# Optimization experiments

Hardware: AMD Instinct MI355X
Metric: run time of the kernel (lower is better)

The kernel has to match this reference:

```python
import jax, jax.numpy as jnp
import numpy as np

B, LS, LT = 64, 64, 64
E, H = 512, 512
VS, VT = 32000, 32000


def setup_inputs() -> dict:
    key = jax.random.key(0)
    ks = jax.random.split(key, 16)
    s = 0.02
    inp = {
        "src": jax.random.randint(ks[0], (B, LS), 0, VS),
        "tgt": jax.random.randint(ks[1], (B, LT), 0, VT),
        # encoder params
        "src_embed": jax.random.normal(ks[2], (VS, E), jnp.float32) * s,
        "enc_Wx": jax.random.normal(ks[3], (E, 4 * H), jnp.float32) * s,   # [i|f|g|o]
        "enc_Wh": jax.random.normal(ks[4], (H, 4 * H), jnp.float32) * s,
        "enc_b": jnp.zeros((4 * H,), jnp.float32),
        # decoder params
        "tgt_embed": jax.random.normal(ks[5], (VT, E), jnp.float32) * s,
        "att_Wh": jax.random.normal(ks[6], (H, H), jnp.float32) * s,
        "att_Ws": jax.random.normal(ks[7], (H, H), jnp.float32) * s,
        "att_v": jax.random.normal(ks[8], (H,), jnp.float32) * s,
        "dec_Wx": jax.random.normal(ks[9], (E + H, 4 * H), jnp.float32) * s,
        "dec_Wh": jax.random.normal(ks[10], (H, 4 * H), jnp.float32) * s,
        "dec_b": jnp.zeros((4 * H,), jnp.float32),
        "h2o_W": jax.random.normal(ks[11], (2 * H, VT), jnp.float32) * s,
        "h2o_b": jnp.zeros((VT,), jnp.float32),
    }
    return inp


def _lstm_step(x, h, c, Wx, Wh, b):
    # x:(B,in), h,c:(B,H). Gates packed as [i|f|g|o] along last dim (same math
    # as 8 separate nn.Linear calls with biases summed).
    z = x @ Wx + h @ Wh + b
    i, f, g, o = jnp.split(z, 4, axis=-1)
    c_new = jax.nn.sigmoid(f) * c + jax.nn.sigmoid(i) * jnp.tanh(g)
    h_new = jax.nn.sigmoid(o) * jnp.tanh(c_new)
    return h_new, c_new


def reference(src, tgt, src_embed, enc_Wx, enc_Wh, enc_b, tgt_embed,
              att_Wh, att_Ws, att_v, dec_Wx, dec_Wh, dec_b, h2o_W, h2o_b):
    Bs = src.shape[0]
    h0 = jnp.zeros((Bs, H), jnp.float32)
    c0 = jnp.zeros((Bs, H), jnp.float32)

    # ---- encoder: scan over source timesteps ----
    src_emb = src_embed[src]                       # (B,Ls,E)
    xs_enc = jnp.swapaxes(src_emb, 0, 1)           # (Ls,B,E)

    def enc_step(carry, x):
        h, c = carry
        h, c = _lstm_step(x, h, c, enc_Wx, enc_Wh, enc_b)
        return (h, c), h

    (h_enc, c_enc), enc_hs = jax.lax.scan(enc_step, (h0, c0), xs_enc)
    enc_hiddens = jnp.swapaxes(enc_hs, 0, 1)       # (B,Ls,H)

    # encoder-side attention projection is decoder-state independent: hoist it
    enc_t = enc_hiddens @ att_Wh                   # (B,Ls,H)

    # ---- decoder: teacher forcing, scan over target timesteps ----
    tgt_emb = tgt_embed[tgt]                       # (B,Lt,E)
    xs_dec = jnp.swapaxes(tgt_emb, 0, 1)           # (Lt,B,E)

    def dec_step(carry, emb):
        h, c = carry
        # Bahdanau additive attention on previous decoder hidden h
        dec_t = h @ att_Ws                                        # (B,H)
        energy = jnp.tanh(enc_t + dec_t[:, None, :]) @ att_v      # (B,Ls)
        attn = jax.nn.softmax(energy, axis=-1)                    # (B,Ls)
        context = jnp.einsum('bs,bsh->bh', attn, enc_hiddens)     # (B,H)
        lstm_in = jnp.concatenate([emb, context], axis=-1)        # (B,E+H)
        h, c = _lstm_step(lstm_in, h, c, dec_Wx, dec_Wh, dec_b)
        logits = jnp.concatenate([h, context], axis=-1) @ h2o_W + h2o_b
        out = jax.nn.log_softmax(logits, axis=-1)                 # (B,Vt)
        return (h, c), out

    _, outs = jax.lax.scan(dec_step, (h_enc, c_enc), xs_dec)      # (Lt,B,Vt)
    return jnp.swapaxes(outs, 0, 1)                               # (B,Lt,Vt)
```

## Files before the change

### kernel.cpp

```cpp
#include <hip/hip_runtime.h>
#include <hip/hip_bf16.h>
#include <math.h>

#define BB 64
#define LL 64
#define EE 512
#define HH 512
#define G4 2048
#define VT 32000
#define RT 4096

typedef unsigned short u16;
typedef unsigned int u32;
typedef unsigned char u8;
typedef __attribute__((ext_vector_type(2))) unsigned int u32x2;
typedef __attribute__((ext_vector_type(8))) unsigned short ushort8;
typedef __attribute__((ext_vector_type(8))) short bf16x8;
typedef __attribute__((ext_vector_type(4))) float f32x4;

__device__ u16   gW2T[(size_t)VT * 1024];
__device__ u16   gEncWxT[G4 * EE];
__device__ u16   gEncWhT[G4 * HH];
__device__ u16   gAttWhT[HH * HH];
__device__ u16   gDecWxTe[G4 * EE];
__device__ u16   gDecWxTc[G4 * HH];
__device__ u16   gDecWhT[G4 * HH];
__device__ u8    gWs8[HH * HH];
__device__ u16   gSrcEmb[RT * EE];
__device__ u16   gTgtEmb[RT * EE];
__device__ float gXWxE[(size_t)RT * G4];
__device__ float gXWxD[(size_t)RT * G4];
__device__ u16   gEncHb[(size_t)RT * HH];
__device__ u16   gEncHb2[(size_t)RT * HH];
__device__ u16   gEncTb[(size_t)RT * HH];
__device__ u16   gHcat[(size_t)RT * 1024];
__device__ float gC[BB * HH];
__device__ float gAv[HH];
__device__ unsigned gFlagE[64];
__device__ unsigned gFlagB[64];
__device__ unsigned gFlagC[64];
__device__ unsigned gStep;

__device__ __forceinline__ u16 f2b(float f) {
    union { float f; unsigned u; } v{f};
    unsigned r = v.u + 0x7fffu + ((v.u >> 16) & 1u);
    return (u16)(r >> 16);
}
__device__ __forceinline__ float b2f(u16 x) {
    union { unsigned u; float f; } v; v.u = ((unsigned)x) << 16; return v.f;
}
__device__ __forceinline__ float sigm(float x) { return 1.f / (1.f + __expf(-x)); }
__device__ __forceinline__ float ftanh(float x) {
    x = fminf(15.f, fmaxf(-15.f, x));
    float e = __expf(2.f * x);
    return (e - 1.f) / (e + 1.f);
}

__device__ unsigned char encf8(float f) {
    union { float f; unsigned u; } v{f};
    unsigned s = (v.u >> 31) << 7;
    float af = fabsf(f);
    if (af < 0.0009765625f) return (unsigned char)s;
    if (af >= 448.f) return (unsigned char)(s | 0x7E);
    if (af < 0.015625f) {
        int q = (int)rintf(af * 512.f);
        if (q >= 8) return (unsigned char)(s | 0x08);
        return (unsigned char)(s | q);
    }
    int e; float m = frexpf(af, &e);
    int E = e - 1 + 7;
    int q = (int)rintf((m * 2.f - 1.f) * 8.f);
    if (q == 8) { E++; q = 0; }
    if (E >= 15) return (unsigned char)(s | 0x7E);
    return (unsigned char)(s | (E << 3) | q);
}
__device__ __forceinline__ float decf8s(unsigned v) {
    unsigned s = v >> 7, e = (v >> 3) & 15, m = v & 7;
    float mag = e ? ldexpf((float)(8 + m), (int)e - 10) : ldexpf((float)m, -9);
    return s ? -mag : mag;
}
#if __has_builtin(__builtin_amdgcn_cvt_f32_fp8)
#define DEC8(w, sel) __builtin_amdgcn_cvt_f32_fp8((int)(w), sel)
#else
#define DEC8(w, sel) decf8s(((w) >> (8 * (sel))) & 0xFFu)
#endif

__device__ __forceinline__ void ld16(const void* addr, bf16x8* a) {
    asm volatile(
        "global_load_dwordx4 %0, %16, off sc0 sc1\n\t"
        "global_load_dwordx4 %1, %16, off offset:64 sc0 sc1\n\t"
        "global_load_dwordx4 %2, %16, off offset:128 sc0 sc1\n\t"
        "global_load_dwordx4 %3, %16, off offset:192 sc0 sc1\n\t"
        "global_load_dwordx4 %4, %16, off offset:256 sc0 sc1\n\t"
        "global_load_dwordx4 %5, %16, off offset:320 sc0 sc1\n\t"
        "global_load_dwordx4 %6, %16, off offset:384 sc0 sc1\n\t"
        "global_load_dwordx4 %7, %16, off offset:448 sc0 sc1\n\t"
        "global_load_dwordx4 %8, %16, off offset:512 sc0 sc1\n\t"
        "global_load_dwordx4 %9, %16, off offset:576 sc0 sc1\n\t"
        "global_load_dwordx4 %10, %16, off offset:640 sc0 sc1\n\t"
        "global_load_dwordx4 %11, %16, off offset:704 sc0 sc1\n\t"
        "global_load_dwordx4 %12, %16, off offset:768 sc0 sc1\n\t"
        "global_load_dwordx4 %13, %16, off offset:832 sc0 sc1\n\t"
        "global_load_dwordx4 %14, %16, off offset:896 sc0 sc1\n\t"
        "global_load_dwordx4 %15, %16, off offset:960 sc0 sc1\n\t"
        "s_waitcnt vmcnt(0)"
        : "=&v"(a[0]), "=&v"(a[1]), "=&v"(a[2]), "=&v"(a[3]),
          "=&v"(a[4]), "=&v"(a[5]), "=&v"(a[6]), "=&v"(a[7]),
          "=&v"(a[8]), "=&v"(a[9]), "=&v"(a[10]), "=&v"(a[11]),
          "=&v"(a[12]), "=&v"(a[13]), "=&v"(a[14]), "=&v"(a[15])
        : "v"(addr) : "memory");
}
__device__ __forceinline__ u32 ld1(const void* addr) {
    u32 r;
    asm volatile("global_load_dword %0, %1, off sc0 sc1\n\ts_waitcnt vmcnt(0)"
                 : "=&v"(r) : "v"(addr) : "memory");
    return r;
}
__device__ __forceinline__ void st8b(void* p, u32x2 v) {
    asm volatile("global_store_dwordx2 %0, %1, off sc0 sc1" :: "v"(p), "v"(v) : "memory");
}
__device__ __forceinline__ void st32b(u32* p, u32 v) {
    asm volatile("global_store_dword %0, %1, off sc0 sc1" :: "v"(p), "v"(v) : "memory");
}

__device__ __forceinline__ void setflag(unsigned* f, unsigned v) {
    asm volatile("s_waitcnt vmcnt(0)" ::: "memory");
    __syncthreads();
    if (threadIdx.x == 0) st32b((u32*)f, v);
}
__device__ __forceinline__ void waitflags(unsigned* flags, int n, unsigned target) {
    if (threadIdx.x < 64) {
        const unsigned* p = flags + (threadIdx.x & (n - 1));
        for (;;) {
            u32 v = ld1(p);
            if (__all(v >= target)) break;
            __builtin_amdgcn_s_sleep(1);
        }
    }
    __syncthreads();
}

__device__ __forceinline__ void g2l16(const u16* g, u16* l) {
    __builtin_amdgcn_global_load_lds(
        (const __attribute__((address_space(1))) unsigned int*)g,
        (__attribute__((address_space(3))) unsigned int*)l, 16, 0, 0);
}
__device__ __forceinline__ void g2l16nt(const u16* g, u16* l) {
    __builtin_amdgcn_global_load_lds(
        (const __attribute__((address_space(1))) unsigned int*)g,
        (__attribute__((address_space(3))) unsigned int*)l, 16, 0, 2);
}

__global__ __launch_bounds__(256) void k_prep(
    const int* __restrict__ src, const int* __restrict__ tgt,
    const float* __restrict__ src_embed, const float* __restrict__ tgt_embed,
    const float* __restrict__ enc_Wx, const float* __restrict__ enc_Wh,
    const float* __restrict__ att_Wh, const float* __restrict__ dec_Wx,
    const float* __restrict__ dec_Wh, const float* __restrict__ att_Ws,
    const float* __restrict__ av) {
    int bx = blockIdx.x, tid = threadIdx.x;
    if (bx < 1344) {
        __shared__ float tile[32][33];
        int tx = tid & 31, ty0 = tid >> 5;
#pragma unroll 1
        for (int q = 0; q < 4; q++) {
            int ti = bx * 4 + q;
            const float* in; u16* outp; int C, rel;
            if (ti < 1024)      { in = enc_Wx;  outp = gEncWxT;  C = 2048; rel = ti; }
            else if (ti < 2048) { in = enc_Wh;  outp = gEncWhT;  C = 2048; rel = ti - 1024; }
            else if (ti < 2304) { in = att_Wh;  outp = gAttWhT;  C = 512;  rel = ti - 2048; }
            else if (ti < 3328) { in = dec_Wx;  outp = gDecWxTe; C = 2048; rel = ti - 2304; }
            else if (ti < 4352) { in = dec_Wx + (size_t)512 * 2048; outp = gDecWxTc; C = 2048; rel = ti - 3328; }
            else                { in = dec_Wh;  outp = gDecWhT;  C = 2048; rel = ti - 4352; }
            int tpr = C / 32;
            int c0 = (rel % tpr) * 32, r0 = (rel / tpr) * 32;
            __syncthreads();
#pragma unroll
            for (int k = 0; k < 4; k++) {
                int ty = ty0 + k * 8;
                tile[ty][tx] = in[(size_t)(r0 + ty) * C + c0 + tx];
            }
            __syncthreads();
#pragma unroll
            for (int k = 0; k < 4; k++) {
                int ty = ty0 + k * 8;
                outp[(size_t)(c0 + ty) * 512 + r0 + tx] = f2b(tile[tx][ty]);
            }
        }
    } else if (bx < 1408) {
        int base = (bx - 1344) * 4096;
        for (int i = tid; i < 4096; i += 256) gWs8[base + i] = encf8(att_Ws[base + i]);
    } else if (bx < 1664) {
        int r0 = (bx - 1408) * 16;
        for (int rr = 0; rr < 16; rr++) {
            int r = r0 + rr, b = r & 63, t = r >> 6;
            int token = src[b * LL + t];
            const float* srow = src_embed + (size_t)token * EE;
            for (int e = tid; e < EE; e += 256)
                gSrcEmb[(size_t)r * EE + e] = f2b(srow[e]);
        }
    } else if (bx < 1920) {
        int r0 = (bx - 1664) * 16;
        for (int rr = 0; rr < 16; rr++) {
            int r = r0 + rr, b = r & 63, t = r >> 6;
            int token = tgt[b * LL + t];
            const float* srow = tgt_embed + (size_t)token * EE;
            for (int e = tid; e < EE; e += 256)
                gTgtEmb[(size_t)r * EE + e] = f2b(srow[e]);
        }
    } else {
        int base = (bx - 1920) * 2048;
        for (int i = tid; i < 2048; i += 256) gC[base + i] = 0.f;
        if (bx == 1920) {
            if (tid < 64) {
                st32b((u32*)(gFlagE + tid), 0u);
                st32b((u32*)(gFlagB + tid), 0u);
                st32b((u32*)(gFlagC + tid), 0u);
            }
            if (tid == 0) st32b((u32*)&gStep, 0u);
            gAv[tid] = av[tid];
            gAv[tid + 256] = av[tid + 256];
        }
    }
}

__global__ __launch_bounds__(256) void k_gemm(int selA, int lda, int selB, int ldb,
                                              int M, int N, int K, int epi,
                                              const float* __restrict__ bias, int selOut) {
    __shared__ u16 sA[128 * 72];
    __shared__ u16 sB[128 * 72];
    const u16* Ag = (selA == 0) ? gSrcEmb : gEncHb;
    const u16* Bg = (selB == 0) ? gEncWxT : gAttWhT;
    float* Cg = gXWxE;

    int tid = threadIdx.x, l = tid & 63, wid = tid >> 6, wr = wid >> 1, wc = wid & 1;
    int ar = l & 15, ak = (l >> 4) * 8;
    int rowM = blockIdx.y * 128, colN = blockIdx.x * 128;
    f32x4 acc[4][4];
#pragma unroll
    for (int m = 0; m < 4; m++)
#pragma unroll
        for (int n = 0; n < 4; n++) acc[m][n] = (f32x4){0.f, 0.f, 0.f, 0.f};

    for (int k0 = 0; k0 < K; k0 += 64) {
#pragma unroll
        for (int it = 0; it < 4; it++) {
            int idx = it * 256 + tid;
            int row = idx >> 3, cc = idx & 7;
            *(ushort8*)(sA + row * 72 + cc * 8) =
                *(const ushort8*)(Ag + (size_t)(rowM + row) * lda + k0 + cc * 8);
            *(ushort8*)(sB + row * 72 + cc * 8) =
                *(const ushort8*)(Bg + (size_t)(colN + row) * ldb + k0 + cc * 8);
        }
        __syncthreads();
#pragma unroll
        for (int ks = 0; ks < 2; ks++) {
            bf16x8 a[4], b[4];
#pragma unroll
            for (int m = 0; m < 4; m++) a[m] = *(const bf16x8*)(sA + (wr * 64 + m * 16 + ar) * 72 + ks * 32 + ak);
#pragma unroll
            for (int n = 0; n < 4; n++) b[n] = *(const bf16x8*)(sB + (wc * 64 + n * 16 + ar) * 72 + ks * 32 + ak);
#pragma unroll
            for (int m = 0; m < 4; m++)
#pragma unroll
                for (int n = 0; n < 4; n++)
                    acc[m][n] = __builtin_amdgcn_mfma_f32_16x16x32_bf16(a[m], b[n], acc[m][n], 0, 0, 0);
        }
        __syncthreads();
    }
    int rb = (l >> 4) * 4;
#pragma unroll
    for (int m = 0; m < 4; m++)
#pragma unroll
        for (int n = 0; n < 4; n++)
#pragma unroll
            for (int ri = 0; ri < 4; ri++) {
                int row = rowM + wr * 64 + m * 16 + rb + ri;
                int col = colN + wc * 64 + n * 16 + ar;
                float v = acc[m][n][ri];
                if (epi == 2) Cg[(size_t)row * N + col] = v + bias[col];
                else gEncTb[(size_t)((row & 63) * 64 + (row >> 6)) * N + col] = f2b(v);
            }
}

__global__ __launch_bounds__(256) void k_encoder(const float* __restrict__ dec_b,
                                                 const float* __restrict__ h2o_W) {
    __shared__ char smem[67584];
    int tid = threadIdx.x, l = tid & 63, wid = tid >> 6;
    int bx = blockIdx.x;
    int ar = l & 15, ak = (l >> 4) * 8, rb = (l >> 4) * 4;
    if (bx < 32) {
        u16* sW = (u16*)smem;
        u16* s_hout = (u16*)(smem + 65536);
        int j = bx;
#pragma unroll
        for (int it = 0; it < 16; it++) {
            int idx = it * 256 + tid;
            int lr = idx >> 6, kc = idx & 63;
            int gcol = (lr >> 4) * 512 + j * 16 + (lr & 15);
            int off = (lr * 1024 + kc * 16) ^ ((lr & 7) << 4);
            *(ushort8*)((char*)sW + off) = *(const ushort8*)(gEncWhT + (size_t)gcol * 512 + kc * 8);
        }
        __syncthreads();
        int arow = wid * 16 + ar, aoff = (l >> 4) * 16;
        int hcol = j * 16 + ar;
        for (int t = 0; t < LL; t++) {
            float xwv[4][4];
#pragma unroll
            for (int ri = 0; ri < 4; ri++) {
                const float* xw = gXWxE + (size_t)(t * BB + wid * 16 + rb + ri) * G4;
#pragma unroll
                for (int g = 0; g < 4; g++) xwv[ri][g] = xw[g * 512 + hcol];
            }
            f32x4 acc[4];
#pragma unroll
            for (int g = 0; g < 4; g++) acc[g] = (f32x4){0.f, 0.f, 0.f, 0.f};
            if (t > 0) {
                waitflags(gFlagE, 32, (unsigned)t);
                bf16x8 af[16];
                ld16((const char*)gEncHb + (size_t)((t - 1) * BB + arow) * 1024 + aoff, af);
#pragma unroll
                for (int kk = 0; kk < 16; kk++) {
                    int k = kk * 32 + ak;
#pragma unroll
                    for (int g = 0; g < 4; g++) {
                        int lr = g * 16 + ar;
                        bf16x8 b = *(const bf16x8*)((char*)sW + ((lr * 1024 + k * 2) ^ ((lr & 7) << 4)));
                        acc[g] = __builtin_amdgcn_mfma_f32_16x16x32_bf16(af[kk], b, acc[g], 0, 0, 0);
                    }
                }
            }
#pragma unroll
            for (int ri = 0; ri < 4; ri++) {
                int row = wid * 16 + rb + ri;
                float zi = acc[0][ri] + xwv[ri][0];
                float zf = acc[1][ri] + xwv[ri][1];
                float zg = acc[2][ri] + xwv[ri][2];
                float zo = acc[3][ri] + xwv[ri][3];
                float co = gC[row * HH + hcol];
                float cn = sigm(zf) * co + sigm(zi) * ftanh(zg);
                float hn = sigm(zo) * ftanh(cn);
                gC[row * HH + hcol] = cn;
                s_hout[row * 16 + ar] = f2b(hn);
            }
            __syncthreads();
            {
                int row = tid >> 2, seg = tid & 3;
                u32x2 v = *(const u32x2*)(s_hout + row * 16 + seg * 4);
                st8b(gEncHb + (size_t)(t * BB + row) * HH + j * 16 + seg * 4, v);
                *(u32x2*)(gEncHb2 + (size_t)(row * LL + t) * HH + j * 16 + seg * 4) = v;
            }
            setflag(gFlagE + j, (unsigned)(t + 1));
        }
    } else if (bx < 96) {
        u16* sA = (u16*)smem;
        u16* sB = (u16*)(smem + 18432);
        int wr = wid >> 1, wc = wid & 1;
        for (int it8 = 0; it8 < 8; it8++) {
            int ti = (bx - 32) * 8 + it8;
            int bxx = ti & 15, byy = ti >> 4;
            int rowM = byy * 128, colN = bxx * 128;
            f32x4 acc[4][4];
#pragma unroll
            for (int m = 0; m < 4; m++)
#pragma unroll
                for (int n = 0; n < 4; n++) acc[m][n] = (f32x4){0.f, 0.f, 0.f, 0.f};
            for (int k0 = 0; k0 < 512; k0 += 64) {
#pragma unroll
                for (int it = 0; it < 4; it++) {
                    int idx = it * 256 + tid;
                    int row = idx >> 3, cc = idx & 7;
                    *(ushort8*)(sA + row * 72 + cc * 8) =
                        *(const ushort8*)(gTgtEmb + (size_t)(rowM + row) * 512 + k0 + cc * 8);
                    *(ushort8*)(sB + row * 72 + cc * 8) =
                        *(const ushort8*)(gDecWxTe + (size_t)(colN + row) * 512 + k0 + cc * 8);
                }
                __syncthreads();
#pragma unroll
                for (int ks = 0; ks < 2; ks++) {
                    bf16x8 a[4], b[4];
#pragma unroll
                    for (int m = 0; m < 4; m++) a[m] = *(const bf16x8*)(sA + (wr * 64 + m * 16 + ar) * 72 + ks * 32 + ak);
#pragma unroll
                    for (int n = 0; n < 4; n++) b[n] = *(const bf16x8*)(sB + (wc * 64 + n * 16 + ar) * 72 + ks * 32 + ak);
#pragma unroll
                    for (int m = 0; m < 4; m++)
#pragma unroll
                        for (int n = 0; n < 4; n++)
                            acc[m][n] = __builtin_amdgcn_mfma_f32_16x16x32_bf16(a[m], b[n], acc[m][n], 0, 0, 0);
                }
                __syncthreads();
            }
#pragma unroll
            for (int m = 0; m < 4; m++)
#pragma unroll
                for (int n = 0; n < 4; n++)
#pragma unroll
                    for (int ri = 0; ri < 4; ri++) {
                        int row = rowM + wr * 64 + m * 16 + rb + ri;
                        int col = colN + wc * 64 + n * 16 + ar;
                        gXWxD[(size_t)row * G4 + col] = acc[m][n][ri] + dec_b[col];
                    }
        }
    } else {
        float (*tile)[33] = (float(*)[33])smem;
        int tx = tid & 31, ty0 = tid >> 5;
        for (int k = 0; k < 200; k++) {
            int ti = (bx - 96) * 200 + k;
            int ct = ti % 1000, rt = ti / 1000;
            int c0 = ct * 32, r0 = rt * 32;
            __syncthreads();
#pragma unroll
            for (int kk = 0; kk < 4; kk++) {
                int ty = ty0 + kk * 8;
                tile[ty][tx] = h2o_W[(size_t)(r0 + ty) * VT + c0 + tx];
            }
            __syncthreads();
#pragma unroll
            for (int kk = 0; kk < 4; kk++) {
                int ty = ty0 + kk * 8;
                gW2T[(size_t)(c0 + ty) * 1024 + r0 + tx] = f2b(tile[tx][ty]);
            }
        }
    }
}

__global__ __launch_bounds__(256) void k_decoder(const float* __restrict__ h2o_b,
                                                 float* __restrict__ out) {
    __shared__ u16 sWh[64 * 512];
    __shared__ u16 sWx[64 * 512];
    __shared__ u16 s_hout[64 * 16];
    __shared__ float s_h[512];
    __shared__ float s_dt[512];
    __shared__ float s_av[512];
    __shared__ float s_att[64];
    __shared__ float s_red[256];
    __shared__ float s_mv[4][520];
    int tid = threadIdx.x, l = tid & 63, wid = tid >> 6;
    int bx = blockIdx.x;
    int ar = l & 15, ak = (l >> 4) * 8, rb = (l >> 4) * 4;
    int arow = wid * 16 + ar, aoff = (l >> 4) * 16;
    if (bx >= 96) {
        u16* csA = sWh;
        u16* csB = sWh + 128 * 64;
        int wr = wid >> 1, wc = wid & 1;
        int srow = wid * 32 + (l >> 3);
        int scol = (l & 7) * 8;
        int ci = bx - 96;
        for (int jt = 0; jt < 50; jt++) {
            int T = ci + 160 * jt;
            int byy = T / 250, bxx = T % 250;
            unsigned tgt = (unsigned)(2 * byy + 2);
            if (tid == 0) {
                while (ld1(&gStep) < tgt) __builtin_amdgcn_s_sleep(32);
            }
            __syncthreads();
            int rowM = byy * 128, colN = bxx * 128;
            f32x4 acc[4][4];
#pragma unroll
            for (int m = 0; m < 4; m++)
#pragma unroll
                for (int n = 0; n < 4; n++) acc[m][n] = (f32x4){0.f, 0.f, 0.f, 0.f};
            for (int k0 = 0; k0 < 1024; k0 += 64) {
#pragma unroll
                for (int c = 0; c < 4; c++) {
                    int r = srow + c * 8;
                    g2l16(gHcat + (size_t)(rowM + r) * 1024 + k0 + scol, csA + r * 64 + scol);
                    g2l16nt(gW2T + (size_t)(colN + r) * 1024 + k0 + scol, csB + r * 64 + scol);
                }
                __syncthreads();
#pragma unroll
                for (int ks = 0; ks < 2; ks++) {
                    bf16x8 a[4], b[4];
#pragma unroll
                    for (int m = 0; m < 4; m++) a[m] = *(const bf16x8*)(csA + (wr * 64 + m * 16 + ar) * 64 + ks * 32 + ak);
#pragma unroll
                    for (int n = 0; n < 4; n++) b[n] = *(const bf16x8*)(csB + (wc * 64 + n * 16 + ar) * 64 + ks * 32 + ak);
#pragma unroll
                    for (int m = 0; m < 4; m++)
#pragma unroll
                        for (int n = 0; n < 4; n++)
                            acc[m][n] = __builtin_amdgcn_mfma_f32_16x16x32_bf16(a[m], b[n], acc[m][n], 0, 0, 0);
                }
                __syncthreads();
            }
#pragma unroll
            for (int m = 0; m < 4; m++)
#pragma unroll
                for (int n = 0; n < 4; n++)
#pragma unroll
                    for (int ri = 0; ri < 4; ri++) {
                        int row = rowM + wr * 64 + m * 16 + rb + ri;
                        int col = colN + wc * 64 + n * 16 + ar;
                        out[(size_t)((row & 63) * 64 + (row >> 6)) * VT + col] = acc[m][n][ri] + h2o_b[col];
                    }
        }
        return;
    }
    if (bx >= 64) {
        int j = bx - 64;
#pragma unroll
        for (int it = 0; it < 16; it++) {
            int idx = it * 256 + tid;
            int lr = idx >> 6, kc = idx & 63;
            int gcol = (lr >> 4) * 512 + j * 16 + (lr & 15);
            int off = (lr * 1024 + kc * 16) ^ ((lr & 7) << 4);
            *(ushort8*)((char*)sWh + off) = *(const ushort8*)(gDecWhT + (size_t)gcol * 512 + kc * 8);
            *(ushort8*)((char*)sWx + off) = *(const ushort8*)(gDecWxTc + (size_t)gcol * 512 + kc * 8);
        }
    } else {
        s_av[tid] = gAv[tid];
        s_av[tid + 256] = gAv[tid + 256];
    }
    __syncthreads();
    for (int t = 0; t < LL; t++) {
        if (bx >= 64) {
            int j = bx - 64;
            int hcol = j * 16 + ar;
            float xwv[4][4];
#pragma unroll
            for (int ri = 0; ri < 4; ri++) {
                const float* xw = gXWxD + (size_t)(t * BB + wid * 16 + rb + ri) * G4;
#pragma unroll
                for (int g = 0; g < 4; g++) xwv[ri][g] = xw[g * 512 + hcol];
            }
            if (t > 0) waitflags(gFlagC, 32, (unsigned)t);
            if (t > 0 && bx == 64 && tid == 0) st32b((u32*)&gStep, (unsigned)t);
            bf16x8 af[16];
            const char* baseA = (t == 0)
                ? ((const char*)gEncHb + (size_t)(63 * BB + arow) * 1024 + aoff)
                : ((const char*)gHcat + (size_t)((t - 1) * BB + arow) * 2048 + aoff);
            ld16(baseA, af);
            f32x4 acc[4];
#pragma unroll
            for (int g = 0; g < 4; g++) acc[g] = (f32x4){0.f, 0.f, 0.f, 0.f};
#pragma unroll
            for (int kk = 0; kk < 16; kk++) {
                int k = kk * 32 + ak;
#pragma unroll
                for (int g = 0; g < 4; g++) {
                    int lr = g * 16 + ar;
                    bf16x8 b = *(const bf16x8*)((char*)sWh + ((lr * 1024 + k * 2) ^ ((lr & 7) << 4)));
                    acc[g] = __builtin_amdgcn_mfma_f32_16x16x32_bf16(af[kk], b, acc[g], 0, 0, 0);
                }
            }
            waitflags(gFlagB, 64, (unsigned)(t + 1));
            bf16x8 cf[16];
            ld16((const char*)gHcat + (size_t)(t * BB + arow) * 2048 + 1024 + aoff, cf);
#pragma unroll
            for (int kk = 0; kk < 16; kk++) {
                int k = kk * 32 + ak;
#pragma unroll
                for (int g = 0; g < 4; g++) {
                    int lr = g * 16 + ar;
                    bf16x8 b = *(const bf16x8*)((char*)sWx + ((lr * 1024 + k * 2) ^ ((lr & 7) << 4)));
                    acc[g] = __builtin_amdgcn_mfma_f32_16x16x32_bf16(cf[kk], b, acc[g], 0, 0, 0);
                }
            }
#pragma unroll
            for (int ri = 0; ri < 4; ri++) {
                int row = wid * 16 + rb + ri;
                float zi = acc[0][ri] + xwv[ri][0];
                float zf = acc[1][ri] + xwv[ri][1];
                float zg = acc[2][ri] + xwv[ri][2];
                float zo = acc[3][ri] + xwv[ri][3];
                float co = gC[row * HH + hcol];
                float cn = sigm(zf) * co + sigm(zi) * ftanh(zg);
                float hn = sigm(zo) * ftanh(cn);
                gC[row * HH + hcol] = cn;
                s_hout[row * 16 + ar] = f2b(hn);
            }
            __syncthreads();
            {
                int row = tid >> 2, seg = tid & 3;
                u32x2 v = *(const u32x2*)(s_hout + row * 16 + seg * 4);
                st8b(gHcat + (size_t)(t * BB + row) * 1024 + j * 16 + seg * 4, v);
            }
            setflag(gFlagC + j, (unsigned)(t + 1));
        } else {
            int b = bx;
            if (t > 0) waitflags(gFlagC, 32, (unsigned)t);
            const char* hb = (t == 0) ? ((const char*)gEncHb + (size_t)(63 * BB + b) * 1024)
                                      : ((const char*)gHcat + (size_t)((t - 1) * BB + b) * 2048);
            u32 hw = ld1(hb + 4 * tid);
            s_h[2 * tid] = b2f((u16)(hw & 0xffff));
            s_h[2 * tid + 1] = b2f((u16)(hw >> 16));
            __syncthreads();
            {
                int c8 = tid & 63, kq = tid >> 6;
                float a8[8];
#pragma unroll
                for (int jj = 0; jj < 8; jj++) a8[jj] = 0.f;
                const u8* wp = gWs8 + (size_t)(kq * 128) * 512 + c8 * 8;
#pragma unroll 4
                for (int i = 0; i < 128; i++) {
                    u32x2 w = *(const u32x2*)(wp + (size_t)i * 512);
                    float hk = s_h[kq * 128 + i];
                    a8[0] += hk * DEC8(w.x, 0);
                    a8[1] += hk * DEC8(w.x, 1);
                    a8[2] += hk * DEC8(w.x, 2);
                    a8[3] += hk * DEC8(w.x, 3);
                    a8[4] += hk * DEC8(w.y, 0);
                    a8[5] += hk * DEC8(w.y, 1);
                    a8[6] += hk * DEC8(w.y, 2);
                    a8[7] += hk * DEC8(w.y, 3);
                }
#pragma unroll
                for (int jj = 0; jj < 8; jj++) s_mv[kq][c8 * 8 + jj] = a8[jj];
            }
            __syncthreads();
            s_dt[tid] = s_mv[0][tid] + s_mv[1][tid] + s_mv[2][tid] + s_mv[3][tid];
            s_dt[tid + 256] = s_mv[0][tid + 256] + s_mv[1][tid + 256] + s_mv[2][tid + 256] + s_mv[3][tid + 256];
            __syncthreads();
            {
                int s = tid >> 2, q = tid & 3;
                const u16* et = gEncTb + (size_t)(b * 64 + s) * 512 + q * 128;
                const float* dtp = s_dt + q * 128;
                const float* avp = s_av + q * 128;
                float p = 0.f;
#pragma unroll
                for (int i = 0; i < 16; i++) {
                    ushort8 ev = *(const ushort8*)(et + i * 8);
#pragma unroll
                    for (int jj = 0; jj < 8; jj++) {
                        int h = i * 8 + jj;
                        p += ftanh(b2f((u16)ev[jj]) + dtp[h]) * avp[h];
                    }
                }
                s_red[tid] = p;
            }
            __syncthreads();
            if (tid < 64) {
                float v = s_red[tid * 4] + s_red[tid * 4 + 1] + s_red[tid * 4 + 2] + s_red[tid * 4 + 3];
                float m = v;
                for (int o = 32; o; o >>= 1) m = fmaxf(m, __shfl_xor(m, o));
                float e = __expf(v - m);
                float ss = e;
                for (int o = 32; o; o >>= 1) ss += __shfl_xor(ss, o);
                s_att[tid] = e / ss;
            }
            __syncthreads();
            int c = tid * 2;
            float c0 = 0.f, c1 = 0.f;
            const u16* eh = gEncHb2 + (size_t)b * LL * HH;
#pragma unroll 8
            for (int s2 = 0; s2 < 64; s2++) {
                float a = s_att[s2];
                u32 w = *(const u32*)(eh + (size_t)s2 * HH + c);
                c0 += a * b2f((u16)(w & 0xffff));
                c1 += a * b2f((u16)(w >> 16));
            }
            u32 cw = (u32)f2b(c0) | ((u32)f2b(c1) << 16);
            st32b((u32*)(gHcat + (size_t)(t * BB + b) * 1024 + 512 + c), cw);
            setflag(gFlagB + b, (unsigned)(t + 1));
        }
    }
    if (bx == 64) {
        waitflags(gFlagC, 32, 64u);
        waitflags(gFlagB, 64, 64u);
        if (tid == 0) st32b((u32*)&gStep, 64u);
    }
}

__global__ __launch_bounds__(256) void k_lsm(float* __restrict__ out) {
    int row = blockIdx.x, tid = threadIdx.x;
    float4* p4 = (float4*)(out + (size_t)row * VT);
    float m = -1e30f, s = 0.f;
    for (int i = tid; i < VT / 4; i += 256) {
        float4 v = p4[i];
        float mx = fmaxf(fmaxf(v.x, v.y), fmaxf(v.z, v.w));
        float mn = fmaxf(m, mx);
        s = s * __expf(m - mn) + __expf(v.x - mn) + __expf(v.y - mn) + __expf(v.z - mn) + __expf(v.w - mn);
        m = mn;
    }
    for (int o = 32; o; o >>= 1) {
        float m2 = __shfl_xor(m, o), s2 = __shfl_xor(s, o);
        float mn = fmaxf(m, m2);
        s = s * __expf(m - mn) + s2 * __expf(m2 - mn);
        m = mn;
    }
    __shared__ float rm[4], rs[4];
    if ((tid & 63) == 0) { rm[tid >> 6] = m; rs[tid >> 6] = s; }
    __syncthreads();
    float mm = fmaxf(fmaxf(rm[0], rm[1]), fmaxf(rm[2], rm[3]));
    float ss = rs[0] * __expf(rm[0] - mm) + rs[1] * __expf(rm[1] - mm) +
               rs[2] * __expf(rm[2] - mm) + rs[3] * __expf(rm[3] - mm);
    float lse = mm + __logf(ss);
    for (int i = tid; i < VT / 4; i += 256) {
        float4 v = p4[i];
        v.x -= lse; v.y -= lse; v.z -= lse; v.w -= lse;
        p4[i] = v;
    }
}

extern "C" void kernel_launch(void* const* d_in, const int* in_sizes, int n_in,
                              void* d_out, int out_size, void* d_ws, size_t ws_size,
                              hipStream_t stream) {
    const int*   src       = (const int*)d_in[0];
    const int*   tgt       = (const int*)d_in[1];
    const float* src_embed = (const float*)d_in[2];
    const float* enc_Wx    = (const float*)d_in[3];
    const float* enc_Wh    = (const float*)d_in[4];
    const float* enc_b     = (const float*)d_in[5];
    const float* tgt_embed = (const float*)d_in[6];
    const float* att_Wh    = (const float*)d_in[7];
    const float* att_Ws    = (const float*)d_in[8];
    const float* att_v     = (const float*)d_in[9];
    const float* dec_Wx    = (const float*)d_in[10];
    const float* dec_Wh    = (const float*)d_in[11];
    const float* dec_b     = (const float*)d_in[12];
    const float* h2o_W     = (const float*)d_in[13];
    const float* h2o_b     = (const float*)d_in[14];
    float* out = (float*)d_out;
    dim3 blk(256);

    k_prep<<<1936, blk, 0, stream>>>(src, tgt, src_embed, tgt_embed,
                                     enc_Wx, enc_Wh, att_Wh, dec_Wx, dec_Wh,
                                     att_Ws, att_v);
    k_gemm<<<dim3(G4 / 128, RT / 128), blk, 0, stream>>>(0, 512, 0, 512, RT, G4, 512, 2, enc_b, 0);
    const float* decb = dec_b;
    const float* h2ow = h2o_W;
    void* eargs[] = { (void*)&decb, (void*)&h2ow };
    hipLaunchCooperativeKernel((const void*)k_encoder, dim3(256), dim3(256), eargs, 0, stream);
    k_gemm<<<dim3(HH / 128, RT / 128), blk, 0, stream>>>(2, 512, 2, 512, RT, HH, 512, 4, nullptr, 2);
    const float* h2ob = h2o_b;
    float* outp = out;
    void* dargs[] = { (void*)&h2ob, (void*)&outp };
    hipLaunchCooperativeKernel((const void*)k_decoder, dim3(256), dim3(256), dargs, 0, stream);
    k_lsm<<<RT, blk, 0, stream>>>(out);
}
```

Before: 2.751 ms.

## Store logits as bf16 scratch and stage log-softmax row in shared memory

The output-projection GEMM now writes bias-added logits as bf16 into a scratch buffer, staged through shared memory so the global stores are coalesced. The log-softmax kernel reads the bf16 row once, keeps it in LDS, and writes the final fp32 output in a single pass instead of reading and rewriting fp32 output twice. This cuts HBM traffic on the large logits tensor. In exchange the logits are rounded to bf16 before normalization, which costs accuracy, and the per-element online softmax update adds extra exp work.

After: 2.762 ms. About the same (+0.4%).

```diff
diff --git a/kernel.cpp b/kernel.cpp
--- a/kernel.cpp
+++ b/kernel.cpp
@@ -34,6 +34,7 @@
 __device__ u16   gEncHb2[(size_t)RT * HH];
 __device__ u16   gEncTb[(size_t)RT * HH];
 __device__ u16   gHcat[(size_t)RT * 1024];
+__device__ u16   gLogB[(size_t)RT * VT];
 __device__ float gC[BB * HH];
 __device__ float gAv[HH];
 __device__ unsigned gFlagE[64];
@@ -443,6 +444,7 @@
     if (bx >= 96) {
         u16* csA = sWh;
         u16* csB = sWh + 128 * 64;
+        u16* stg = sWx;
         int wr = wid >> 1, wc = wid & 1;
         int srow = wid * 32 + (l >> 3);
         int scol = (l & 7) * 8;
@@ -490,10 +492,19 @@
                 for (int n = 0; n < 4; n++)
 #pragma unroll
                     for (int ri = 0; ri < 4; ri++) {
-                        int row = rowM + wr * 64 + m * 16 + rb + ri;
-                        int col = colN + wc * 64 + n * 16 + ar;
-                        out[(size_t)((row & 63) * 64 + (row >> 6)) * VT + col] = acc[m][n][ri] + h2o_b[col];
+                        int lrow = wr * 64 + m * 16 + rb + ri;
+                        int lcol = wc * 64 + n * 16 + ar;
+                        stg[lrow * 128 + lcol] = f2b(acc[m][n][ri] + h2o_b[colN + lcol]);
                     }
+            __syncthreads();
+            for (int i = tid; i < 128 * 32; i += 256) {
+                int lrow = i >> 5, seg = i & 31;
+                int grow = rowM + lrow;
+                int orow = (grow & 63) * 64 + (grow >> 6);
+                u32x2 v = *(const u32x2*)(stg + lrow * 128 + seg * 4);
+                st8b(gLogB + (size_t)orow * VT + colN + seg * 4, v);
+            }
+            __syncthreads();
         }
         return;
     }
@@ -663,15 +674,21 @@
 }
 
 __global__ __launch_bounds__(256) void k_lsm(float* __restrict__ out) {
+    __shared__ u16 srow[VT];
+    __shared__ float rm[4], rs[4];
     int row = blockIdx.x, tid = threadIdx.x;
-    float4* p4 = (float4*)(out + (size_t)row * VT);
+    const u16* src = gLogB + (size_t)row * VT;
     float m = -1e30f, s = 0.f;
-    for (int i = tid; i < VT / 4; i += 256) {
-        float4 v = p4[i];
-        float mx = fmaxf(fmaxf(v.x, v.y), fmaxf(v.z, v.w));
-        float mn = fmaxf(m, mx);
-        s = s * __expf(m - mn) + __expf(v.x - mn) + __expf(v.y - mn) + __expf(v.z - mn) + __expf(v.w - mn);
-        m = mn;
+    for (int i = tid; i < VT / 8; i += 256) {
+        ushort8 v = *(const ushort8*)(src + i * 8);
+        *(ushort8*)(srow + i * 8) = v;
+#pragma unroll
+        for (int j = 0; j < 8; j++) {
+            float f = b2f((u16)v[j]);
+            float mn = fmaxf(m, f);
+            s = s * __expf(m - mn) + __expf(f - mn);
+            m = mn;
+        }
     }
     for (int o = 32; o; o >>= 1) {
         float m2 = __shfl_xor(m, o), s2 = __shfl_xor(s, o);
@@ -679,17 +696,20 @@
         s = s * __expf(m - mn) + s2 * __expf(m2 - mn);
         m = mn;
     }
-    __shared__ float rm[4], rs[4];
     if ((tid & 63) == 0) { rm[tid >> 6] = m; rs[tid >> 6] = s; }
     __syncthreads();
     float mm = fmaxf(fmaxf(rm[0], rm[1]), fmaxf(rm[2], rm[3]));
     float ss = rs[0] * __expf(rm[0] - mm) + rs[1] * __expf(rm[1] - mm) +
                rs[2] * __expf(rm[2] - mm) + rs[3] * __expf(rm[3] - mm);
     float lse = mm + __logf(ss);
+    float* op = out + (size_t)row * VT;
     for (int i = tid; i < VT / 4; i += 256) {
-        float4 v = p4[i];
-        v.x -= lse; v.y -= lse; v.z -= lse; v.w -= lse;
-        p4[i] = v;
+        float4 o;
+        o.x = b2f(srow[i * 4 + 0]) - lse;
+        o.y = b2f(srow[i * 4 + 1]) - lse;
+        o.z = b2f(srow[i * 4 + 2]) - lse;
+        o.w = b2f(srow[i * 4 + 3]) - lse;
+        *(float4*)(op + i * 4) = o;
     }
 }
 
```
